# Kernel tuning notes

Measured on AMD Instinct MI355X. Metric: run time of the kernel, lower is better.

Reference implementation:

```python
import jax, jax.numpy as jnp
import numpy as np

B, C_IN, H, W = 4096, 3, 32, 32
C1, C2, K = 32, 64, 3
FC1, NCLS = 256, 10


def _extract_patches(x):
    # x: (B, C, H, W) -> patches (B, C, K*K, H, W), 3x3 neighborhoods, pad=1
    xp = jnp.pad(x, ((0, 0), (0, 0), (1, 1), (1, 1)))
    shifts = [xp[:, :, i:i + H, j:j + W] for i in range(K) for j in range(K)]
    return jnp.stack(shifts, axis=2)


def _maxpool2(x):
    b, c, h, w = x.shape
    return x.reshape(b, c, h // 2, 2, w // 2, 2).max(axis=(3, 5))


def setup_inputs() -> dict:
    key = jax.random.key(0)
    ks = jax.random.split(key, 9)
    # kaiming-ish scales
    s_lc = np.sqrt(2.0 / (C_IN * K * K)).astype(np.float32)
    s_cv = np.sqrt(2.0 / (C1 * K * K)).astype(np.float32)
    s_f1 = np.sqrt(2.0 / (C2 * 8 * 8)).astype(np.float32)
    s_f2 = np.sqrt(2.0 / FC1).astype(np.float32)
    return {
        "x": jax.random.normal(ks[0], (B, C_IN, H, W), dtype=jnp.float32),
        # unshared per-location weights: (O, C, K*K, H, W)
        "w_lc": jax.random.normal(ks[1], (C1, C_IN, K * K, H, W), dtype=jnp.float32) * s_lc,
        "b_lc": jnp.zeros((C1, H, W), dtype=jnp.float32),
        "w_conv": jax.random.normal(ks[2], (C2, C1, K, K), dtype=jnp.float32) * s_cv,
        "b_conv": jnp.zeros((C2,), dtype=jnp.float32),
        "w_fc1": jax.random.normal(ks[3], (FC1, C2 * 8 * 8), dtype=jnp.float32) * s_f1,
        "b_fc1": jnp.zeros((FC1,), dtype=jnp.float32),
        "w_fc2": jax.random.normal(ks[4], (NCLS, FC1), dtype=jnp.float32) * s_f2,
        "b_fc2": jnp.zeros((NCLS,), dtype=jnp.float32),
    }


def reference(x, w_lc, b_lc, w_conv, b_conv, w_fc1, b_fc1, w_fc2, b_fc2):
    # locally connected layer: per-(i,j) unshared 3x3 filters
    patches = _extract_patches(x)                                  # (B, C, 9, H, W)
    y = jnp.einsum('bckij,ockij->boij', patches, w_lc) + b_lc[None]  # (B, C1, H, W)
    y = jax.nn.relu(y)
    y = _maxpool2(y)                                               # (B, C1, 16, 16)
    # standard 3x3 conv, padding SAME
    y = jax.lax.conv_general_dilated(
        y, w_conv, window_strides=(1, 1), padding='SAME',
        dimension_numbers=('NCHW', 'OIHW', 'NCHW'))
    y = jax.nn.relu(y + b_conv[None, :, None, None])
    y = _maxpool2(y)                                               # (B, C2, 8, 8)
    y = y.reshape(y.shape[0], -1)                                  # (B, C2*8*8)
    y = jax.nn.relu(y @ w_fc1.T + b_fc1)
    return y @ w_fc2.T + b_fc2                                     # (B, num_classes)
```

## Files before the change

### kernel.cpp

```cpp
#include <hip/hip_runtime.h>

typedef short s16x8 __attribute__((ext_vector_type(8)));
typedef float f32x4 __attribute__((ext_vector_type(4)));
typedef unsigned short u16x4 __attribute__((ext_vector_type(4)));

static __device__ __forceinline__ unsigned short f2bf(float f) {
    union { float f; unsigned u; } v; v.f = f;
    unsigned r = v.u + 0x7FFF + ((v.u >> 16) & 1);
    return (unsigned short)(r >> 16);
}
static __device__ __forceinline__ float quad_fmax(float a) {
    int ai = __builtin_bit_cast(int, a);
    int s1 = __builtin_amdgcn_mov_dpp(ai, 0xB1, 0xF, 0xF, true);
    a = fmaxf(a, __builtin_bit_cast(float, s1));
    ai = __builtin_bit_cast(int, a);
    int s2 = __builtin_amdgcn_mov_dpp(ai, 0x4E, 0xF, 0xF, true);
    return fmaxf(a, __builtin_bit_cast(float, s2));
}

__global__ __launch_bounds__(256) void k_prep(
    const float* __restrict__ w_lc, const float* __restrict__ b_lc,
    const float* __restrict__ w_conv, const float* __restrict__ w_fc1,
    unsigned short* __restrict__ btab, unsigned short* __restrict__ wt_g,
    unsigned short* __restrict__ Wb)
{
    const int t = threadIdx.x, bx = blockIdx.x;
    if (bx < 1024) {
        const int gid = bx * 256 + t;
        const int k8 = gid & 7;
        const int nn = (gid >> 3) & 127;
        const int jp = (gid >> 10) & 15;
        const int pr = gid >> 14;
        const int o = nn >> 2, ih = (nn >> 1) & 1, jc = nn & 1;
        const int row = 2 * pr + ih, col = 2 * jp + jc;
        unsigned v32[8];
        #pragma unroll
        for (int e = 0; e < 8; ++e) {
            const int k = k8 * 8 + e;
            float v = 0.f;
            if (k < 48) {
                const int c = k >> 4, rr = (k >> 2) & 3, cf = k & 3;
                const int di = rr - ih, dj = cf - jc;
                if ((unsigned)di < 3u && (unsigned)dj < 3u)
                    v = w_lc[((o * 3 + c) * 9 + di * 3 + dj) * 1024 + row * 32 + col];
            } else if (k == 63) {
                v = b_lc[o * 1024 + row * 32 + col];
            }
            v32[e] = f2bf(v);
        }
        uint4 w;
        w.x = v32[0] | (v32[1] << 16);
        w.y = v32[2] | (v32[3] << 16);
        w.z = v32[4] | (v32[5] << 16);
        w.w = v32[6] | (v32[7] << 16);
        *(uint4*)&btab[(size_t)gid * 8] = w;
    } else if (bx < 1088) {
        const float4* wf4 = (const float4*)w_fc1;
        for (int f = t; f < 4096; f += 256) {
            const int idx = (bx - 1024) * 4096 + f;
            const float4 v = wf4[idx];
            u16x4 o = { f2bf(v.x), f2bf(v.y), f2bf(v.z), f2bf(v.w) };
            *(u16x4*)&Wb[idx * 4] = o;
        }
    } else {
        for (int i = t; i < 9 * 64 * 40; i += 256) wt_g[i] = 0;
        __syncthreads();
        for (int i = t; i < 64 * 32 * 9; i += 256) {
            const int oc = i / 288;
            const int rem = i - oc * 288;
            const int ic = rem / 9;
            const int kk = rem - ic * 9;
            wt_g[(kk * 64 + oc) * 40 + ic] = f2bf(w_conv[i]);
        }
    }
}

__global__ __launch_bounds__(256) void k_lc(
    const float* __restrict__ x,
    const unsigned short* __restrict__ btab,
    unsigned short* __restrict__ y1g)
{
    __shared__ unsigned short xb_raw[8 + 12 * 67 * 34 + 8];
    __shared__ __align__(16) unsigned short pbuf[64][40];
    const int t = threadIdx.x;
    const int ib = blockIdx.x >> 4;
    const int pr = blockIdx.x & 15;
    const int img0 = ib * 64;
    unsigned short* xbp = xb_raw + 8;

    for (int f = t; f < (8 + 12 * 67 * 34 + 8) / 2; f += 256) ((int*)xb_raw)[f] = 0;
    __syncthreads();
    #pragma unroll
    for (int i = 0; i < 24; ++i) {
        const int f = t + i * 256;
        const int img = f / 96;
        const int rem = f - img * 96;
        const int c = rem >> 5, rr = (rem >> 3) & 3, cf = rem & 7;
        const int xrow = 2 * pr - 1 + rr;
        if ((unsigned)xrow < 32u) {
            const float4 v = *(const float4*)&x[
                ((size_t)(img0 + img) * 3 + c) * 1024 + xrow * 32 + cf * 4];
            const unsigned w0 = (unsigned)f2bf(v.x) | ((unsigned)f2bf(v.y) << 16);
            const unsigned w1 = (unsigned)f2bf(v.z) | ((unsigned)f2bf(v.w) << 16);
            const int imgl = (img & 15) + (img >> 4) * 17;
            const int sa = ((c * 4 + rr) * 67 + imgl) * 34 + cf * 4;
            *(unsigned*)&xbp[sa] = w0;
            *(unsigned*)&xbp[sa + 2] = w1;
        }
    }
    __syncthreads();

    const int lane = t & 63, wv = t >> 6;
    const int lc = lane & 15, lg = lane >> 4;
    const unsigned short* bpb = btab + (((size_t)pr * 16) * 128 + wv * 32) * 64;

    const int r1a = (8 + lg * 2 > 11) ? 11 : 8 + lg * 2;
    const int r1b = (9 + lg * 2 > 11) ? 11 : 9 + lg * 2;

    unsigned short* ybase = y1g + (((size_t)(img0 + lane) * 256) + pr * 16) * 32 + wv * 8;

#define ABUILD(wout, row0, row1, mbase, colb2, biasfix)                        \
    {                                                                          \
        const int rows_[2] = { row0, row1 };                                   \
        _Pragma("unroll")                                                      \
        for (int rI = 0; rI < 2; ++rI) {                                       \
            const int base = (rows_[rI] * 67 + (mbase)) * 34 + (colb2);        \
            const unsigned d0 = *(const unsigned*)&xbp[base];                  \
            const unsigned d1 = *(const unsigned*)&xbp[base + 2];              \
            const unsigned d2 = *(const unsigned*)&xbp[base + 4];              \
            wout[rI * 2 + 0] = (unsigned)(((((unsigned long long)d1) << 32) | d0) >> 16); \
            wout[rI * 2 + 1] = (unsigned)(((((unsigned long long)d2) << 32) | d1) >> 16); \
        }                                                                      \
        if (biasfix && lg == 3) wout[3] = 0x3F800000u;                         \
    }

    for (int jp = 0; jp < 16; ++jp) {
        const int colb2 = jp * 2 - 2;
        const unsigned short* bp = bpb + (size_t)jp * (128 * 64);
        const s16x8 B0 = *(const s16x8*)&bp[lc * 64 + lg * 8];
        const s16x8 B1 = *(const s16x8*)&bp[(16 + lc) * 64 + lg * 8];
        const s16x8 B2 = *(const s16x8*)&bp[lc * 64 + 32 + lg * 8];
        const s16x8 B3 = *(const s16x8*)&bp[(16 + lc) * 64 + 32 + lg * 8];

        #pragma unroll
        for (int mh = 0; mh < 4; ++mh) {
            const int mbase = mh * 17 + lc;
            unsigned wa[4], wb[4];
            ABUILD(wa, lg * 2, lg * 2 + 1, mbase, colb2, 0)
            ABUILD(wb, r1a, r1b, mbase, colb2, 1)
            uint4 ai = { wa[0], wa[1], wa[2], wa[3] };
            uint4 bi = { wb[0], wb[1], wb[2], wb[3] };
            const s16x8 a0 = __builtin_bit_cast(s16x8, ai);
            const s16x8 a1 = __builtin_bit_cast(s16x8, bi);

            f32x4 acc[2];
            {
                f32x4 z = {0.f, 0.f, 0.f, 0.f};
                acc[0] = z; acc[1] = z;
            }
            acc[0] = __builtin_amdgcn_mfma_f32_16x16x32_bf16(a0, B0, acc[0], 0, 0, 0);
            acc[1] = __builtin_amdgcn_mfma_f32_16x16x32_bf16(a0, B1, acc[1], 0, 0, 0);
            acc[0] = __builtin_amdgcn_mfma_f32_16x16x32_bf16(a1, B2, acc[0], 0, 0, 0);
            acc[1] = __builtin_amdgcn_mfma_f32_16x16x32_bf16(a1, B3, acc[1], 0, 0, 0);

            #pragma unroll
            for (int nf = 0; nf < 2; ++nf) {
                f32x4 v = acc[nf];
                #pragma unroll
                for (int q = 0; q < 4; ++q) v[q] = quad_fmax(v[q]);
                const float sel = (lc & 2) ? ((lc & 1) ? v[3] : v[2])
                                           : ((lc & 1) ? v[1] : v[0]);
                const float m = fmaxf(sel, 0.f);
                pbuf[mh * 16 + lg * 4 + (lc & 3)][wv * 8 + nf * 4 + (lc >> 2)] = f2bf(m);
            }
        }
        *(s16x8*)&ybase[(size_t)jp * 32] = *(const s16x8*)&pbuf[lane][wv * 8];
    }
#undef ABUILD
}

__global__ __launch_bounds__(256, 3) void k_conv(
    const unsigned short* __restrict__ y1g,
    const unsigned short* __restrict__ wt_g,
    const float* __restrict__ b_conv,
    unsigned short* __restrict__ p2)
{
    __shared__ __align__(16) unsigned short y1t[18][18][40];
    __shared__ __align__(16) unsigned short pbuf[4][1024];
    const int t = threadIdx.x;
    const int img = blockIdx.x;

    {
        const s16x8 z = {0, 0, 0, 0, 0, 0, 0, 0};
        unsigned short* p = &y1t[0][0][0];
        for (int i = t * 8; i < 18 * 18 * 40; i += 2048) *(s16x8*)(p + i) = z;
    }
    __syncthreads();
    {
        const int prr = t >> 4, pcc = t & 15;
        const unsigned short* src = y1g + ((size_t)img * 256 + t) * 32;
        unsigned short* d = &y1t[prr + 1][pcc + 1][0];
        #pragma unroll
        for (int ch = 0; ch < 4; ++ch)
            *(s16x8*)(d + ch * 8) = *(const s16x8*)(src + ch * 8);
    }
    __syncthreads();

    const int w = t >> 6, lane = t & 63;
    const int lc = lane & 15, lg = lane >> 4;

    f32x4 acc[4][4];
    #pragma unroll
    for (int mf = 0; mf < 4; ++mf)
        #pragma unroll
        for (int nf = 0; nf < 4; ++nf) {
            f32x4 zz = {0.f, 0.f, 0.f, 0.f};
            acc[mf][nf] = zz;
        }
    #pragma unroll
    for (int kk = 0; kk < 9; ++kk) {
        const int di = kk / 3, dj = kk % 3;
        s16x8 a[4], bb[4];
        #pragma unroll
        for (int nf = 0; nf < 4; ++nf)
            bb[nf] = *(const s16x8*)&wt_g[(kk * 64 + nf * 16 + lc) * 40 + lg * 8];
        #pragma unroll
        for (int mf = 0; mf < 4; ++mf)
            a[mf] = *(const s16x8*)&y1t[w * 4 + mf + di][lc + dj][lg * 8];
        #pragma unroll
        for (int mf = 0; mf < 4; ++mf)
            #pragma unroll
            for (int nf = 0; nf < 4; ++nf)
                acc[mf][nf] = __builtin_amdgcn_mfma_f32_16x16x32_bf16(
                    a[mf], bb[nf], acc[mf][nf], 0, 0, 0);
    }
    #pragma unroll
    for (int mfp = 0; mfp < 2; ++mfp) {
        #pragma unroll
        for (int nf = 0; nf < 4; ++nf) {
            const f32x4 u = acc[mfp * 2][nf], v = acc[mfp * 2 + 1][nf];
            const float bbv = b_conv[nf * 16 + lc];
            float q0 = fmaxf(fmaxf(u[0], u[1]), fmaxf(v[0], v[1]));
            float q1 = fmaxf(fmaxf(u[2], u[3]), fmaxf(v[2], v[3]));
            q0 = fmaxf(q0 + bbv, 0.f);
            q1 = fmaxf(q1 + bbv, 0.f);
            *(unsigned*)&pbuf[w][(nf * 16 + lc) * 16 + mfp * 8 + lg * 2] =
                (unsigned)f2bf(q0) | ((unsigned)f2bf(q1) << 16);
        }
    }
    #pragma unroll
    for (int jj = 0; jj < 2; ++jj) {
        const int u8 = jj * 64 + lane;
        const int oc = u8 >> 1, s = (u8 & 1) * 8;
        const s16x8 val = *(const s16x8*)&pbuf[w][u8 * 8];
        *(s16x8*)&p2[((size_t)img * 64 + oc) * 64 + w * 16 + s] = val;
    }
}

__global__ __launch_bounds__(256) void k_fc1(
    const unsigned short* __restrict__ A,
    const unsigned short* __restrict__ Wb,
    const float* __restrict__ bias, float* __restrict__ fc1p)
{
    __shared__ __align__(16) unsigned short As[64][72];
    __shared__ __align__(16) unsigned short Bs[32][72];
    const int t = threadIdx.x;
    const int m0 = blockIdx.x * 64, n0 = blockIdx.y * 32;
    const int z = blockIdx.z;
    const int w = t >> 6, lane = t & 63;
    const int lc = lane & 15, lg = lane >> 4;
    f32x4 acc[2];
    {
        const float bv0 = (z == 0) ? bias[n0 + lc] : 0.f;
        const float bv1 = (z == 0) ? bias[n0 + 16 + lc] : 0.f;
        f32x4 a0 = {bv0, bv0, bv0, bv0}, a1 = {bv1, bv1, bv1, bv1};
        acc[0] = a0; acc[1] = a1;
    }
    const int kbase = z * 2048;
    for (int k0 = kbase; k0 < kbase + 2048; k0 += 64) {
        {
            const int r0 = t >> 3, ch0 = (t & 7) * 8;
            const int id1 = t + 256;
            const int r1 = id1 >> 3, ch1 = (id1 & 7) * 8;
            *(s16x8*)&As[r0][ch0] = *(const s16x8*)&A[(size_t)(m0 + r0) * 4096 + k0 + ch0];
            *(s16x8*)&As[r1][ch1] = *(const s16x8*)&A[(size_t)(m0 + r1) * 4096 + k0 + ch1];
            const int rb = t >> 3, cb = (t & 7) * 8;
            *(s16x8*)&Bs[rb][cb] = *(const s16x8*)&Wb[(size_t)(n0 + rb) * 4096 + k0 + cb];
        }
        __syncthreads();
        #pragma unroll
        for (int kh = 0; kh < 2; ++kh) {
            const s16x8 a  = *(const s16x8*)&As[w * 16 + lc][kh * 32 + lg * 8];
            const s16x8 b0 = *(const s16x8*)&Bs[lc][kh * 32 + lg * 8];
            const s16x8 b1 = *(const s16x8*)&Bs[16 + lc][kh * 32 + lg * 8];
            acc[0] = __builtin_amdgcn_mfma_f32_16x16x32_bf16(a, b0, acc[0], 0, 0, 0);
            acc[1] = __builtin_amdgcn_mfma_f32_16x16x32_bf16(a, b1, acc[1], 0, 0, 0);
        }
        __syncthreads();
    }
    #pragma unroll
    for (int nf = 0; nf < 2; ++nf) {
        const int n = n0 + nf * 16 + lc;
        #pragma unroll
        for (int q = 0; q < 4; ++q) {
            const int m = m0 + w * 16 + lg * 4 + q;
            fc1p[((size_t)z * 4096 + m) * 256 + n] = acc[nf][q];
        }
    }
}

__global__ __launch_bounds__(320) void k_fc2(
    const float* __restrict__ fc1p, const float* __restrict__ Wt,
    const float* __restrict__ bias, float* __restrict__ out)
{
    const int t = threadIdx.x;
    const int r = blockIdx.x * 32 + t / 10;
    const int n = t % 10;
    const float4* a0 = (const float4*)(fc1p + (size_t)r * 256);
    const float4* a1 = (const float4*)(fc1p + (size_t)(4096 + r) * 256);
    const float4* w = (const float4*)(Wt + (size_t)n * 256);
    float acc = bias[n];
    #pragma unroll 8
    for (int k = 0; k < 64; ++k) {
        const float4 u = a0[k], v = a1[k], wv = w[k];
        acc += fmaxf(u.x + v.x, 0.f) * wv.x + fmaxf(u.y + v.y, 0.f) * wv.y +
               fmaxf(u.z + v.z, 0.f) * wv.z + fmaxf(u.w + v.w, 0.f) * wv.w;
    }
    out[(size_t)r * 10 + n] = acc;
}

extern "C" void kernel_launch(void* const* d_in, const int* in_sizes, int n_in,
                              void* d_out, int out_size, void* d_ws, size_t ws_size,
                              hipStream_t stream)
{
    const float* x      = (const float*)d_in[0];
    const float* w_lc   = (const float*)d_in[1];
    const float* b_lc   = (const float*)d_in[2];
    const float* w_conv = (const float*)d_in[3];
    const float* b_conv = (const float*)d_in[4];
    const float* w_fc1  = (const float*)d_in[5];
    const float* b_fc1  = (const float*)d_in[6];
    const float* w_fc2  = (const float*)d_in[7];
    const float* b_fc2  = (const float*)d_in[8];
    float* out = (float*)d_out;

    unsigned short* p2b  = (unsigned short*)d_ws;
    unsigned short* btab = (unsigned short*)((char*)d_ws + 16777216);
    unsigned short* y1g  = (unsigned short*)((char*)d_ws + 33554432);
    float*          fc1p = (float*)((char*)d_ws + 33554432);
    unsigned short* Wb   = (unsigned short*)((char*)d_ws + 67108864);
    unsigned short* wt_g = (unsigned short*)((char*)d_ws + 69206016);

    k_prep<<<1089, 256, 0, stream>>>(w_lc, b_lc, w_conv, w_fc1, btab, wt_g, Wb);
    for (int half = 0; half < 2; ++half) {
        k_lc<<<512, 256, 0, stream>>>(x + (size_t)half * 2048 * 3072, btab, y1g);
        k_conv<<<2048, 256, 0, stream>>>(y1g, wt_g, b_conv,
                                         p2b + (size_t)half * 2048 * 4096);
    }
    k_fc1<<<dim3(64, 8, 2), 256, 0, stream>>>(p2b, Wb, b_fc1, fc1p);
    k_fc2<<<128, 320, 0, stream>>>(fc1p, w_fc2, b_fc2, out);
}
```

Before: 189.9 us.

## Pack pooled LC outputs to bf16 before max and widen fc1 N tile

In the locally connected kernel, the epilogue now converts accumulators to packed bf16 first and does the 2x2 quad max and ReLU with packed 16-bit integer max in inline assembly, which cuts the DPP/max instruction count. This relies on signed-int16 ordering matching bf16 ordering, which does not hold for pairs of negative values, though ReLU hides most of those cases. Separately, the fc1 GEMM tile grows from 64x32 to 64x64 per block, with half as many blocks, so each A tile is reused across four MFMA columns and A is read from global memory fewer times.

```diff
diff --git a/kernel.cpp b/kernel.cpp
--- a/kernel.cpp
+++ b/kernel.cpp
@@ -8,14 +8,6 @@
     union { float f; unsigned u; } v; v.f = f;
     unsigned r = v.u + 0x7FFF + ((v.u >> 16) & 1);
     return (unsigned short)(r >> 16);
-}
-static __device__ __forceinline__ float quad_fmax(float a) {
-    int ai = __builtin_bit_cast(int, a);
-    int s1 = __builtin_amdgcn_mov_dpp(ai, 0xB1, 0xF, 0xF, true);
-    a = fmaxf(a, __builtin_bit_cast(float, s1));
-    ai = __builtin_bit_cast(int, a);
-    int s2 = __builtin_amdgcn_mov_dpp(ai, 0x4E, 0xF, 0xF, true);
-    return fmaxf(a, __builtin_bit_cast(float, s2));
 }
 
 __global__ __launch_bounds__(256) void k_prep(
@@ -112,6 +104,8 @@
 
     const int lane = t & 63, wv = t >> 6;
     const int lc = lane & 15, lg = lane >> 4;
+    const int shamt = (lc & 1) << 4;
+    const unsigned long long m2 = __ballot(lc & 2);
     const unsigned short* bpb = btab + (((size_t)pr * 16) * 128 + wv * 32) * 64;
 
     const int r1a = (8 + lg * 2 > 11) ? 11 : 8 + lg * 2;
@@ -165,13 +159,28 @@
 
             #pragma unroll
             for (int nf = 0; nf < 2; ++nf) {
-                f32x4 v = acc[nf];
-                #pragma unroll
-                for (int q = 0; q < 4; ++q) v[q] = quad_fmax(v[q]);
-                const float sel = (lc & 2) ? ((lc & 1) ? v[3] : v[2])
-                                           : ((lc & 1) ? v[1] : v[0]);
-                const float m = fmaxf(sel, 0.f);
-                pbuf[mh * 16 + lg * 4 + (lc & 3)][wv * 8 + nf * 4 + (lc >> 2)] = f2bf(m);
+                unsigned res, p1t, q0t, q1t;
+                asm("v_cvt_pk_bf16_f32 %0, %4, %5\n\t"
+                    "v_cvt_pk_bf16_f32 %1, %6, %7\n\t"
+                    "s_nop 1\n\t"
+                    "v_mov_b32 %2, %0 quad_perm:[1,0,3,2] row_mask:0xf bank_mask:0xf\n\t"
+                    "v_mov_b32 %3, %1 quad_perm:[1,0,3,2] row_mask:0xf bank_mask:0xf\n\t"
+                    "v_pk_max_i16 %0, %0, %2\n\t"
+                    "v_pk_max_i16 %1, %1, %3\n\t"
+                    "s_nop 1\n\t"
+                    "v_mov_b32 %2, %0 quad_perm:[2,3,0,1] row_mask:0xf bank_mask:0xf\n\t"
+                    "v_mov_b32 %3, %1 quad_perm:[2,3,0,1] row_mask:0xf bank_mask:0xf\n\t"
+                    "v_pk_max_i16 %0, %0, %2\n\t"
+                    "v_pk_max_i16 %1, %1, %3\n\t"
+                    "v_cndmask_b32 %0, %0, %1, %9\n\t"
+                    "v_alignbit_b32 %0, %0, %0, %8\n\t"
+                    "v_pk_max_i16 %0, %0, 0"
+                    : "=&v"(res), "=&v"(p1t), "=&v"(q0t), "=&v"(q1t)
+                    : "v"(acc[nf][0]), "v"(acc[nf][1]),
+                      "v"(acc[nf][2]), "v"(acc[nf][3]),
+                      "v"(shamt), "s"(m2));
+                pbuf[mh * 16 + lg * 4 + (lc & 3)][wv * 8 + nf * 4 + (lc >> 2)] =
+                    (unsigned short)res;
             }
         }
         *(s16x8*)&ybase[(size_t)jp * 32] = *(const s16x8*)&pbuf[lane][wv * 8];
@@ -263,43 +272,40 @@
     const float* __restrict__ bias, float* __restrict__ fc1p)
 {
     __shared__ __align__(16) unsigned short As[64][72];
-    __shared__ __align__(16) unsigned short Bs[32][72];
+    __shared__ __align__(16) unsigned short Bs[64][72];
     const int t = threadIdx.x;
-    const int m0 = blockIdx.x * 64, n0 = blockIdx.y * 32;
+    const int m0 = blockIdx.x * 64, n0 = blockIdx.y * 64;
     const int z = blockIdx.z;
     const int w = t >> 6, lane = t & 63;
     const int lc = lane & 15, lg = lane >> 4;
-    f32x4 acc[2];
-    {
-        const float bv0 = (z == 0) ? bias[n0 + lc] : 0.f;
-        const float bv1 = (z == 0) ? bias[n0 + 16 + lc] : 0.f;
-        f32x4 a0 = {bv0, bv0, bv0, bv0}, a1 = {bv1, bv1, bv1, bv1};
-        acc[0] = a0; acc[1] = a1;
+    f32x4 acc[4];
+    #pragma unroll
+    for (int nf = 0; nf < 4; ++nf) {
+        const float bv = (z == 0) ? bias[n0 + nf * 16 + lc] : 0.f;
+        f32x4 a0 = {bv, bv, bv, bv};
+        acc[nf] = a0;
     }
     const int kbase = z * 2048;
+    const int r0 = t >> 3, ch0 = (t & 7) * 8;
     for (int k0 = kbase; k0 < kbase + 2048; k0 += 64) {
-        {
-            const int r0 = t >> 3, ch0 = (t & 7) * 8;
-            const int id1 = t + 256;
-            const int r1 = id1 >> 3, ch1 = (id1 & 7) * 8;
-            *(s16x8*)&As[r0][ch0] = *(const s16x8*)&A[(size_t)(m0 + r0) * 4096 + k0 + ch0];
-            *(s16x8*)&As[r1][ch1] = *(const s16x8*)&A[(size_t)(m0 + r1) * 4096 + k0 + ch1];
-            const int rb = t >> 3, cb = (t & 7) * 8;
-            *(s16x8*)&Bs[rb][cb] = *(const s16x8*)&Wb[(size_t)(n0 + rb) * 4096 + k0 + cb];
-        }
+        *(s16x8*)&As[r0][ch0]      = *(const s16x8*)&A[(size_t)(m0 + r0) * 4096 + k0 + ch0];
+        *(s16x8*)&As[r0 + 32][ch0] = *(const s16x8*)&A[(size_t)(m0 + r0 + 32) * 4096 + k0 + ch0];
+        *(s16x8*)&Bs[r0][ch0]      = *(const s16x8*)&Wb[(size_t)(n0 + r0) * 4096 + k0 + ch0];
+        *(s16x8*)&Bs[r0 + 32][ch0] = *(const s16x8*)&Wb[(size_t)(n0 + r0 + 32) * 4096 + k0 + ch0];
         __syncthreads();
         #pragma unroll
         for (int kh = 0; kh < 2; ++kh) {
-            const s16x8 a  = *(const s16x8*)&As[w * 16 + lc][kh * 32 + lg * 8];
-            const s16x8 b0 = *(const s16x8*)&Bs[lc][kh * 32 + lg * 8];
-            const s16x8 b1 = *(const s16x8*)&Bs[16 + lc][kh * 32 + lg * 8];
-            acc[0] = __builtin_amdgcn_mfma_f32_16x16x32_bf16(a, b0, acc[0], 0, 0, 0);
-            acc[1] = __builtin_amdgcn_mfma_f32_16x16x32_bf16(a, b1, acc[1], 0, 0, 0);
+            const s16x8 a = *(const s16x8*)&As[w * 16 + lc][kh * 32 + lg * 8];
+            #pragma unroll
+            for (int nf = 0; nf < 4; ++nf) {
+                const s16x8 b = *(const s16x8*)&Bs[nf * 16 + lc][kh * 32 + lg * 8];
+                acc[nf] = __builtin_amdgcn_mfma_f32_16x16x32_bf16(a, b, acc[nf], 0, 0, 0);
+            }
         }
         __syncthreads();
     }
     #pragma unroll
-    for (int nf = 0; nf < 2; ++nf) {
+    for (int nf = 0; nf < 4; ++nf) {
         const int n = n0 + nf * 16 + lc;
         #pragma unroll
         for (int q = 0; q < 4; ++q) {
@@ -357,6 +363,6 @@
         k_conv<<<2048, 256, 0, stream>>>(y1g, wt_g, b_conv,
                                          p2b + (size_t)half * 2048 * 4096);
     }
-    k_fc1<<<dim3(64, 8, 2), 256, 0, stream>>>(p2b, Wb, b_fc1, fc1p);
+    k_fc1<<<dim3(64, 4, 2), 256, 0, stream>>>(p2b, Wb, b_fc1, fc1p);
     k_fc2<<<128, 320, 0, stream>>>(fc1p, w_fc2, b_fc2, out);
 }
```

After: 200.3 us. 1.05x slower.
